# Kernel tuning notes

Measured on AMD Instinct MI355X. Metric: run time of the kernel, lower is better.

## Reference

```python
import jax, jax.numpy as jnp
import numpy as np

N_NODES = 100000
N_EDGES = 400000
F_IN = 128
HEADS = 4
C1 = 64   # conv1 out per head
C2 = 128  # conv2 out per head
G = 2048  # num graphs
FP = 2048
HID = 64
NEG_SLOPE = 0.2


def _gat_conv(x, edge_index, W, a_src, a_dst, b, heads, ch):
    """PyG-style GATConv with self-loops, concat=True."""
    n = x.shape[0]
    loops = jnp.arange(n, dtype=edge_index.dtype)
    src = jnp.concatenate([edge_index[0], loops])
    dst = jnp.concatenate([edge_index[1], loops])
    h = (x @ W).reshape(n, heads, ch)                      # [N,H,C]
    e_src = jnp.sum(h * a_src, axis=-1)                    # [N,H]
    e_dst = jnp.sum(h * a_dst, axis=-1)                    # [N,H]
    logits = jax.nn.leaky_relu(e_src[src] + e_dst[dst], NEG_SLOPE)  # [E,H]
    m = jax.ops.segment_max(logits, dst, num_segments=n)   # per-dst max
    p = jnp.exp(logits - m[dst])
    denom = jax.ops.segment_sum(p, dst, num_segments=n)
    alpha = p / denom[dst]                                 # [E,H]
    out = jax.ops.segment_sum(h[src] * alpha[:, :, None], dst, num_segments=n)
    return out.reshape(n, heads * ch) + b


def setup_inputs() -> dict:
    key = jax.random.key(0)
    ks = jax.random.split(key, 16)
    s = 0.05
    inp = {
        "x": jax.random.normal(ks[0], (N_NODES, F_IN), jnp.float32),
        "edge_index": jax.random.randint(ks[1], (2, N_EDGES), 0, N_NODES, jnp.int32),
        "batch": jnp.sort(jax.random.randint(ks[2], (N_NODES,), 0, G, jnp.int32)),
        "fp": jax.random.normal(ks[3], (G, FP), jnp.float32),
        "W1": jax.random.normal(ks[4], (F_IN, HEADS * C1), jnp.float32) * s,
        "a_src1": jax.random.normal(ks[5], (HEADS, C1), jnp.float32) * s,
        "a_dst1": jax.random.normal(ks[6], (HEADS, C1), jnp.float32) * s,
        "b1": jnp.zeros((HEADS * C1,), jnp.float32),
        "W2": jax.random.normal(ks[7], (HEADS * C1, HEADS * C2), jnp.float32) * s,
        "a_src2": jax.random.normal(ks[8], (HEADS, C2), jnp.float32) * s,
        "a_dst2": jax.random.normal(ks[9], (HEADS, C2), jnp.float32) * s,
        "b2": jnp.zeros((HEADS * C2,), jnp.float32),
        "Wfp": jax.random.normal(ks[10], (FP, HID), jnp.float32) * s,
        "bfp": jnp.zeros((HID,), jnp.float32),
        "Wfc1": jax.random.normal(ks[11], (HEADS * C2 + HID, HID), jnp.float32) * s,
        "bfc1": jnp.zeros((HID,), jnp.float32),
        "Wfc2": jax.random.normal(ks[12], (HID, 1), jnp.float32) * s,
        "bfc2": jnp.zeros((1,), jnp.float32),
    }
    return inp


def reference(x, edge_index, batch, fp, W1, a_src1, a_dst1, b1, W2, a_src2, a_dst2, b2,
              Wfp, bfp, Wfc1, bfc1, Wfc2, bfc2):
    h = _gat_conv(x, edge_index, W1, a_src1, a_dst1, b1, HEADS, C1)
    h = jax.nn.elu(h)
    h = _gat_conv(h, edge_index, W2, a_src2, a_dst2, b2, HEADS, C2)
    h = jax.nn.elu(h)
    # global mean pool over graphs
    sums = jax.ops.segment_sum(h, batch, num_segments=G)
    counts = jax.ops.segment_sum(jnp.ones((h.shape[0], 1), h.dtype), batch, num_segments=G)
    pooled = sums / jnp.maximum(counts, 1.0)               # [G, 512]
    fph = fp @ Wfp + bfp                                   # [G, 64]
    z = jnp.concatenate([pooled, fph], axis=1)             # [G, 576]
    z = jax.nn.relu(z @ Wfc1 + bfc1)
    # dropout is identity in eval mode
    return z @ Wfc2 + bfc2                                 # [G, 1]
```

## Files before the change

### kernel.cpp

```cpp
#include <hip/hip_runtime.h>
#include <math.h>

#define NEG_SLOPE 0.2f

typedef __attribute__((ext_vector_type(8))) short bf16x8;
typedef __attribute__((ext_vector_type(4))) float f32x4;

__device__ __forceinline__ float b2f(short s) {
  return __uint_as_float(((unsigned int)(unsigned short)s) << 16);
}
__device__ __forceinline__ unsigned short f2b_rne(float f) {
  unsigned int u = __float_as_uint(f);
  u = (u + 0x7FFF + ((u >> 16) & 1)) >> 16;
  return (unsigned short)u;
}

__global__ void cvt_f2b(const float* __restrict__ in, unsigned short* __restrict__ out, size_t n)
{
  size_t i = (size_t)blockIdx.x * 256 + threadIdx.x;
  size_t stride = (size_t)gridDim.x * 256;
  for (; i < n; i += stride) out[i] = f2b_rne(in[i]);
}

__global__ void transpose_f2b(const float* __restrict__ W, unsigned short* __restrict__ WT,
                              int K, int N)
{
  int idx = blockIdx.x * 256 + threadIdx.x;
  if (idx < K * N) {
    int k = idx / N, n = idx - k * N;
    WT[(size_t)n * K + k] = f2b_rne(W[idx]);
  }
}

template<int EMODE>
__global__ __launch_bounds__(256) void gemm_mfma(
    const unsigned short* __restrict__ A, const unsigned short* __restrict__ BT,
    unsigned short* __restrict__ Cout, int M, int N, int K,
    const float* __restrict__ a_src, const float* __restrict__ a_dst,
    float* __restrict__ es, float* __restrict__ ed, int nh)
{
  const int LDT = 40;
  __shared__ unsigned short As[128 * 40];
  __shared__ unsigned short Bs[128 * 40];
  const int tid  = threadIdx.x;
  const int wave = tid >> 6;
  const int lane = tid & 63;
  const int ln   = lane & 15;
  const int quad = lane >> 4;
  const int wr0  = (wave >> 1) * 64;
  const int wc0  = (wave & 1) * 64;
  const int bm   = blockIdx.y * 128;
  const int bn   = blockIdx.x * 128;
  const int srow  = tid >> 2;
  const int skoff = (tid & 3) * 8;

  f32x4 acc[4][4];
  const f32x4 z4 = {0.f, 0.f, 0.f, 0.f};
#pragma unroll
  for (int i = 0; i < 4; ++i)
#pragma unroll
    for (int j = 0; j < 4; ++j) acc[i][j] = z4;

  const bf16x8 zb8 = {0, 0, 0, 0, 0, 0, 0, 0};
  bf16x8 pa[2] = {zb8, zb8}, pb[2] = {zb8, zb8};
  bf16x8 na[2] = {zb8, zb8}, nb[2] = {zb8, zb8};
#pragma unroll
  for (int p = 0; p < 2; ++p) {
    int r = srow + p * 64;
    pa[p] = (bm + r < M) ? *(const bf16x8*)(A + (size_t)(bm + r) * K + skoff) : zb8;
    pb[p] = *(const bf16x8*)(BT + (size_t)(bn + r) * K + skoff);
  }

  for (int k0 = 0; k0 < K; k0 += 32) {
#pragma unroll
    for (int p = 0; p < 2; ++p) {
      int r = srow + p * 64;
      *(bf16x8*)(&As[r * LDT + skoff]) = pa[p];
      *(bf16x8*)(&Bs[r * LDT + skoff]) = pb[p];
    }
    __syncthreads();
    if (k0 + 32 < K) {
      int kn = k0 + 32;
#pragma unroll
      for (int p = 0; p < 2; ++p) {
        int r = srow + p * 64;
        na[p] = (bm + r < M) ? *(const bf16x8*)(A + (size_t)(bm + r) * K + kn + skoff) : zb8;
        nb[p] = *(const bf16x8*)(BT + (size_t)(bn + r) * K + kn + skoff);
      }
    }
    bf16x8 af[4], bfv[4];
#pragma unroll
    for (int i = 0; i < 4; ++i)
      af[i] = *(const bf16x8*)(&As[(wr0 + i * 16 + ln) * LDT + quad * 8]);
#pragma unroll
    for (int j = 0; j < 4; ++j)
      bfv[j] = *(const bf16x8*)(&Bs[(wc0 + j * 16 + ln) * LDT + quad * 8]);
#pragma unroll
    for (int i = 0; i < 4; ++i)
#pragma unroll
      for (int j = 0; j < 4; ++j)
        acc[i][j] = __builtin_amdgcn_mfma_f32_16x16x32_bf16(af[i], bfv[j], acc[i][j], 0, 0, 0);
    __syncthreads();
#pragma unroll
    for (int p = 0; p < 2; ++p) { pa[p] = na[p]; pb[p] = nb[p]; }
  }

#pragma unroll
  for (int i = 0; i < 4; ++i) {
#pragma unroll
    for (int r = 0; r < 4; ++r) {
      int row = bm + wr0 + i * 16 + quad * 4 + r;
      if (row >= M) continue;
#pragma unroll
      for (int j = 0; j < 4; ++j) {
        int col = bn + wc0 + j * 16 + ln;
        Cout[(size_t)row * N + col] = f2b_rne(acc[i][j][r]);
      }
    }
  }

  float asv[4], adv[4];
#pragma unroll
  for (int j = 0; j < 4; ++j) {
    int col = bn + wc0 + j * 16 + ln;
    asv[j] = a_src[col];
    adv[j] = a_dst[col];
  }
  if (EMODE == 64) {
    const int head = (bn + wc0) >> 6;
#pragma unroll
    for (int i = 0; i < 4; ++i) {
#pragma unroll
      for (int r = 0; r < 4; ++r) {
        float ps = 0.f, pd = 0.f;
#pragma unroll
        for (int j = 0; j < 4; ++j) {
          ps = fmaf(acc[i][j][r], asv[j], ps);
          pd = fmaf(acc[i][j][r], adv[j], pd);
        }
        for (int off = 8; off; off >>= 1) {
          ps += __shfl_down(ps, off, 16);
          pd += __shfl_down(pd, off, 16);
        }
        if (ln == 0) {
          int row = bm + wr0 + i * 16 + quad * 4 + r;
          if (row < M) {
            es[(size_t)row * nh + head] = ps;
            ed[(size_t)row * nh + head] = pd;
          }
        }
      }
    }
  } else {
    float* esp = (float*)As;
    float* edp = esp + 256;
#pragma unroll
    for (int i = 0; i < 4; ++i) {
#pragma unroll
      for (int r = 0; r < 4; ++r) {
        float ps = 0.f, pd = 0.f;
#pragma unroll
        for (int j = 0; j < 4; ++j) {
          ps = fmaf(acc[i][j][r], asv[j], ps);
          pd = fmaf(acc[i][j][r], adv[j], pd);
        }
        for (int off = 8; off; off >>= 1) {
          ps += __shfl_down(ps, off, 16);
          pd += __shfl_down(pd, off, 16);
        }
        if (ln == 0) {
          int rl = wr0 + i * 16 + quad * 4 + r;
          esp[rl * 2 + (wc0 >> 6)] = ps;
          edp[rl * 2 + (wc0 >> 6)] = pd;
        }
      }
    }
    __syncthreads();
    if (tid < 128) {
      int row = bm + tid;
      if (row < M) {
        int head = bn >> 7;
        es[(size_t)row * nh + head] = esp[tid * 2] + esp[tid * 2 + 1];
        ed[(size_t)row * nh + head] = edp[tid * 2] + edp[tid * 2 + 1];
      }
    }
  }
}

__global__ __launch_bounds__(256) void gemm_mfma_n64(
    const unsigned short* __restrict__ A, int lda,
    const unsigned short* __restrict__ BT, int ldb,
    float* __restrict__ Cp, int M, int kchunk)
{
  const int LDT = 72;
  __shared__ unsigned short As[128 * 72];
  __shared__ unsigned short Bs[64 * 72];
  const int tid  = threadIdx.x;
  const int wave = tid >> 6;
  const int lane = tid & 63;
  const int ln   = lane & 15;
  const int quad = lane >> 4;
  const int ks   = blockIdx.x;
  const int bm   = blockIdx.y * 128;
  const int k_beg = ks * kchunk;
  const int k_end = k_beg + kchunk;
  const int arow = tid >> 1;
  const int akb  = (tid & 1) * 32;
  const int brow = tid >> 2;
  const int bkb  = (tid & 3) * 16;

  f32x4 acc[2][4];
  const f32x4 z4 = {0.f, 0.f, 0.f, 0.f};
#pragma unroll
  for (int i = 0; i < 2; ++i)
#pragma unroll
    for (int j = 0; j < 4; ++j) acc[i][j] = z4;

  for (int k0 = k_beg; k0 < k_end; k0 += 64) {
    const unsigned short* ap = A + (size_t)(bm + arow) * lda + k0 + akb;
#pragma unroll
    for (int q = 0; q < 4; ++q)
      *(bf16x8*)(&As[arow * LDT + akb + q * 8]) = *(const bf16x8*)(ap + q * 8);
    const unsigned short* bp = BT + (size_t)brow * ldb + k0 + bkb;
#pragma unroll
    for (int q = 0; q < 2; ++q)
      *(bf16x8*)(&Bs[brow * LDT + bkb + q * 8]) = *(const bf16x8*)(bp + q * 8);
    __syncthreads();
#pragma unroll
    for (int kk = 0; kk < 2; ++kk) {
      bf16x8 af[2], bfv[4];
#pragma unroll
      for (int i = 0; i < 2; ++i)
        af[i] = *(const bf16x8*)(&As[(wave * 32 + i * 16 + ln) * LDT + kk * 32 + quad * 8]);
#pragma unroll
      for (int j = 0; j < 4; ++j)
        bfv[j] = *(const bf16x8*)(&Bs[(j * 16 + ln) * LDT + kk * 32 + quad * 8]);
#pragma unroll
      for (int i = 0; i < 2; ++i)
#pragma unroll
        for (int j = 0; j < 4; ++j)
          acc[i][j] = __builtin_amdgcn_mfma_f32_16x16x32_bf16(af[i], bfv[j], acc[i][j], 0, 0, 0);
    }
    __syncthreads();
  }
#pragma unroll
  for (int i = 0; i < 2; ++i)
#pragma unroll
    for (int r = 0; r < 4; ++r) {
      int row = bm + wave * 32 + i * 16 + quad * 4 + r;
#pragma unroll
      for (int j = 0; j < 4; ++j)
        Cp[((size_t)ks * M + row) * 64 + j * 16 + ln] = acc[i][j][r];
    }
}

__global__ void fp_finish(const float* __restrict__ Cp, int ksplit, int M,
                          const float* __restrict__ bfp,
                          unsigned short* __restrict__ zb)
{
  const int g = blockIdx.x;
  const int j = threadIdx.x;
  float s = bfp[j];
  for (int ks = 0; ks < ksplit; ++ks) s += Cp[((size_t)ks * M + g) * 64 + j];
  zb[(size_t)g * 576 + 512 + j] = f2b_rne(s);
}

__global__ void mlp_finish(const float* __restrict__ Cp, int ksplit, int M,
                           const float* __restrict__ bfc1,
                           const float* __restrict__ Wfc2, const float* __restrict__ bfc2,
                           float* __restrict__ out)
{
  const int g = blockIdx.x;
  const int j = threadIdx.x;
  float s = bfc1[j];
  for (int ks = 0; ks < ksplit; ++ks) s += Cp[((size_t)ks * M + g) * 64 + j];
  s = s > 0.f ? s : 0.f;
  float term = s * Wfc2[j];
  for (int off = 32; off; off >>= 1) term += __shfl_down(term, off, 64);
  if (j == 0) out[g] = term + bfc2[0];
}

__global__ void count_deg(const int* __restrict__ ei, int E, int* __restrict__ deg)
{
  int e = blockIdx.x * 256 + threadIdx.x;
  if (e < E) atomicAdd(&deg[ei[E + e]], 1);
}

__global__ void fill_csr(const int* __restrict__ ei, int E, int* __restrict__ cursor,
                         const int* __restrict__ rowptr, int* __restrict__ csr_src)
{
  int e = blockIdx.x * 256 + threadIdx.x;
  if (e < E) {
    int d = ei[E + e];
    int pos = atomicAdd(&cursor[d], 1);
    csr_src[rowptr[d] + pos] = ei[e];
  }
}

__global__ void count_graph(const int* __restrict__ batch, int N, int* __restrict__ gcnt)
{
  int i = blockIdx.x * 256 + threadIdx.x;
  if (i < N) atomicAdd(&gcnt[batch[i]], 1);
}

__global__ void scan_p1(const int* __restrict__ vals, int n, int* __restrict__ bsum)
{
  __shared__ int red[256];
  int base = blockIdx.x * 1024;
  int t = threadIdx.x;
  int s = 0;
#pragma unroll
  for (int i = 0; i < 4; ++i) {
    int idx = base + i * 256 + t;
    if (idx < n) s += vals[idx];
  }
  red[t] = s;
  __syncthreads();
  for (int off = 128; off; off >>= 1) {
    if (t < off) red[t] += red[t + off];
    __syncthreads();
  }
  if (t == 0) bsum[blockIdx.x] = red[0];
}

__global__ void scan_p2(const int* __restrict__ bsum, int* __restrict__ bpre,
                        int nb, int* __restrict__ rowptr, int n)
{
  __shared__ int tmp[128];
  int t = threadIdx.x;
  int v = (t < nb) ? bsum[t] : 0;
  tmp[t] = v;
  __syncthreads();
  for (int off = 1; off < 128; off <<= 1) {
    int add = (t >= off) ? tmp[t - off] : 0;
    __syncthreads();
    tmp[t] += add;
    __syncthreads();
  }
  if (t < nb) bpre[t] = tmp[t] - v;
  if (t == 127) rowptr[n] = tmp[127];
}

__global__ void scan_p3(const int* __restrict__ vals, const int* __restrict__ bpre,
                        int n, int* __restrict__ rowptr)
{
  __shared__ int tmp[256];
  int t = threadIdx.x;
  int base = blockIdx.x * 1024 + t * 4;
  int v[4]; int s = 0;
#pragma unroll
  for (int i = 0; i < 4; ++i) {
    int idx = base + i;
    v[i] = (idx < n) ? vals[idx] : 0;
    s += v[i];
  }
  tmp[t] = s;
  __syncthreads();
  for (int off = 1; off < 256; off <<= 1) {
    int add = (t >= off) ? tmp[t - off] : 0;
    __syncthreads();
    tmp[t] += add;
    __syncthreads();
  }
  int run = bpre[blockIdx.x] + tmp[t] - s;
#pragma unroll
  for (int i = 0; i < 4; ++i) {
    int idx = base + i;
    if (idx < n) rowptr[idx] = run;
    run += v[i];
  }
}

__global__ void alpha_kernel(const float* __restrict__ es, const float* __restrict__ ed,
                             const int* __restrict__ rowptr, const int* __restrict__ csr_src,
                             float* __restrict__ w_csr, float* __restrict__ wself,
                             int N, int nh)
{
  int idx = blockIdx.x * 256 + threadIdx.x;
  if (idx >= N * nh) return;
  const int dst = idx / nh;
  const int h = idx - dst * nh;
  const float edh = ed[(size_t)dst * nh + h];
  const int beg = rowptr[dst], end = rowptr[dst + 1];
  float sum = 0.f;
  for (int e = beg; e < end; ++e) {
    int s = csr_src[e];
    float l = es[(size_t)s * nh + h] + edh;
    l = l >= 0.f ? l : NEG_SLOPE * l;
    float w = expf(l);
    w_csr[(size_t)e * nh + h] = w;
    sum += w;
  }
  float ls = es[(size_t)dst * nh + h] + edh;
  ls = ls >= 0.f ? ls : NEG_SLOPE * ls;
  float wsl = expf(ls);
  sum += wsl;
  const float inv = 1.0f / sum;
  for (int e = beg; e < end; ++e) w_csr[(size_t)e * nh + h] *= inv;
  wself[(size_t)dst * nh + h] = wsl * inv;
}

__global__ __launch_bounds__(256) void aggregate_b(
    const unsigned short* __restrict__ h,
    const float* __restrict__ w_csr, const float* __restrict__ wself,
    const int* __restrict__ rowptr, const int* __restrict__ csr_src,
    const float* __restrict__ bias, unsigned short* __restrict__ out,
    int N, int nh, int C)
{
  const int HC = nh * C;
  const int CH8 = HC >> 3;
  const int dpb = 256 / CH8;
  const int grp = threadIdx.x / CH8;
  const int lane = threadIdx.x - grp * CH8;
  const int dst = blockIdx.x * dpb + grp;
  if (dst >= N) return;
  const int ch = lane << 3;
  const int head = ch / C;
  const int beg = rowptr[dst], end = rowptr[dst + 1];
  float acc[8] = {0.f, 0.f, 0.f, 0.f, 0.f, 0.f, 0.f, 0.f};
  int e = beg;
  for (; e + 1 < end; e += 2) {
    int s0 = csr_src[e], s1 = csr_src[e + 1];
    float a0 = w_csr[(size_t)e * nh + head];
    float a1 = w_csr[(size_t)(e + 1) * nh + head];
    bf16x8 h0 = *(const bf16x8*)(h + (size_t)s0 * HC + ch);
    bf16x8 h1 = *(const bf16x8*)(h + (size_t)s1 * HC + ch);
#pragma unroll
    for (int r = 0; r < 8; ++r) acc[r] = fmaf(a0, b2f(h0[r]), acc[r]);
#pragma unroll
    for (int r = 0; r < 8; ++r) acc[r] = fmaf(a1, b2f(h1[r]), acc[r]);
  }
  if (e < end) {
    int s0 = csr_src[e];
    float a0 = w_csr[(size_t)e * nh + head];
    bf16x8 h0 = *(const bf16x8*)(h + (size_t)s0 * HC + ch);
#pragma unroll
    for (int r = 0; r < 8; ++r) acc[r] = fmaf(a0, b2f(h0[r]), acc[r]);
  }
  {
    float a = wself[(size_t)dst * nh + head];
    bf16x8 hv = *(const bf16x8*)(h + (size_t)dst * HC + ch);
#pragma unroll
    for (int r = 0; r < 8; ++r) acc[r] = fmaf(a, b2f(hv[r]), acc[r]);
  }
  bf16x8 o;
#pragma unroll
  for (int r = 0; r < 8; ++r) {
    float v = acc[r] + bias[ch + r];
    v = v > 0.f ? v : (expf(v) - 1.0f);
    o[r] = (short)f2b_rne(v);
  }
  *(bf16x8*)(out + (size_t)dst * HC + ch) = o;
}

__global__ __launch_bounds__(256) void agg_pool(
    const unsigned short* __restrict__ h,
    const float* __restrict__ w_csr, const float* __restrict__ wself,
    const int* __restrict__ rowptr, const int* __restrict__ csr_src,
    const float* __restrict__ bias, const int* __restrict__ grp,
    unsigned short* __restrict__ zb)
{
  const int g = blockIdx.x;
  const int wave = threadIdx.x >> 6;
  const int lane = threadIdx.x & 63;
  const int ch = lane << 3;
  const int head = lane >> 4;
  const int gbeg = grp[g], gend = grp[g + 1];
  float bch[8];
#pragma unroll
  for (int r = 0; r < 8; ++r) bch[r] = bias[ch + r];
  float pool[8] = {0.f, 0.f, 0.f, 0.f, 0.f, 0.f, 0.f, 0.f};

  for (int node = gbeg + wave; node < gend; node += 4) {
    const int beg = rowptr[node], end = rowptr[node + 1];
    float acc[8] = {0.f, 0.f, 0.f, 0.f, 0.f, 0.f, 0.f, 0.f};
    int e = beg;
    for (; e + 1 < end; e += 2) {
      int s0 = csr_src[e], s1 = csr_src[e + 1];
      float a0 = w_csr[(size_t)e * 4 + head];
      float a1 = w_csr[(size_t)(e + 1) * 4 + head];
      bf16x8 h0 = *(const bf16x8*)(h + (size_t)s0 * 512 + ch);
      bf16x8 h1 = *(const bf16x8*)(h + (size_t)s1 * 512 + ch);
#pragma unroll
      for (int r = 0; r < 8; ++r) acc[r] = fmaf(a0, b2f(h0[r]), acc[r]);
#pragma unroll
      for (int r = 0; r < 8; ++r) acc[r] = fmaf(a1, b2f(h1[r]), acc[r]);
    }
    if (e < end) {
      int s0 = csr_src[e];
      float a0 = w_csr[(size_t)e * 4 + head];
      bf16x8 h0 = *(const bf16x8*)(h + (size_t)s0 * 512 + ch);
#pragma unroll
      for (int r = 0; r < 8; ++r) acc[r] = fmaf(a0, b2f(h0[r]), acc[r]);
    }
    {
      float a = wself[(size_t)node * 4 + head];
      bf16x8 hv = *(const bf16x8*)(h + (size_t)node * 512 + ch);
#pragma unroll
      for (int r = 0; r < 8; ++r) acc[r] = fmaf(a, b2f(hv[r]), acc[r]);
    }
#pragma unroll
    for (int r = 0; r < 8; ++r) {
      float v = acc[r] + bch[r];
      v = v > 0.f ? v : (expf(v) - 1.0f);
      pool[r] += v;
    }
  }

  __shared__ float red[4][512];
#pragma unroll
  for (int r = 0; r < 8; ++r) red[wave][ch + r] = pool[r];
  __syncthreads();
  const float inv = 1.0f / (float)max(gend - gbeg, 1);
#pragma unroll
  for (int k = 0; k < 2; ++k) {
    int c = threadIdx.x + k * 256;
    float s = (red[0][c] + red[1][c]) + (red[2][c] + red[3][c]);
    zb[(size_t)g * 576 + c] = f2b_rne(s * inv);
  }
}

extern "C" void kernel_launch(void* const* d_in, const int* in_sizes, int n_in,
                              void* d_out, int out_size, void* d_ws, size_t ws_size,
                              hipStream_t stream)
{
  const float* x      = (const float*)d_in[0];
  const int*   ei     = (const int*)d_in[1];
  const int*   batch  = (const int*)d_in[2];
  const float* fp     = (const float*)d_in[3];
  const float* W1     = (const float*)d_in[4];
  const float* a_src1 = (const float*)d_in[5];
  const float* a_dst1 = (const float*)d_in[6];
  const float* b1     = (const float*)d_in[7];
  const float* W2     = (const float*)d_in[8];
  const float* a_src2 = (const float*)d_in[9];
  const float* a_dst2 = (const float*)d_in[10];
  const float* b2     = (const float*)d_in[11];
  const float* Wfp    = (const float*)d_in[12];
  const float* bfp    = (const float*)d_in[13];
  const float* Wfc1   = (const float*)d_in[14];
  const float* bfc1   = (const float*)d_in[15];
  const float* Wfc2   = (const float*)d_in[16];
  const float* bfc2   = (const float*)d_in[17];
  float* out = (float*)d_out;

  const int NN = in_sizes[0] / 128;
  const int E  = in_sizes[1] / 2;
  const int G  = in_sizes[3] / 2048;
  const int FIN = 128, H = 4, C1 = 64, C2 = 128;
  const int HC1 = H * C1;
  const int HC2 = H * C2;
  const int KFP = in_sizes[3] / G;
  const int KZ  = HC2 + 64;
  const int KS_FP = 16;
  const int KS_Z  = 9;

  char* base = (char*)d_ws;
  size_t off = 0;
  auto alloc = [&](size_t bytes) {
    char* p = base + off; off += (bytes + 255) & ~(size_t)255; return p;
  };
  size_t xb_sz  = ((size_t)NN * FIN * 2 + 255) & ~(size_t)255;
  size_t h1b_sz = (size_t)NN * HC1 * 2;
  size_t h2b_sz = (size_t)NN * HC2 * 2;
  size_t rA = xb_sz + h1b_sz; if (h2b_sz > rA) rA = h2b_sz;
  char* RA = alloc(rA);
  unsigned short* xb  = (unsigned short*)RA;
  unsigned short* h1b = (unsigned short*)(RA + xb_sz);
  unsigned short* h2b = (unsigned short*)RA;
  size_t fpb_sz  = ((size_t)G * KFP * 2 + 255) & ~(size_t)255;
  size_t cpfp_sz = (size_t)KS_FP * G * 64 * 4;
  size_t agg1_sz = (size_t)NN * HC1 * 2;
  size_t rB = fpb_sz + cpfp_sz; if (agg1_sz > rB) rB = agg1_sz;
  char* RB = alloc(rB);
  unsigned short* fpb   = (unsigned short*)RB;
  float*          Cp_fp = (float*)(RB + fpb_sz);
  unsigned short* agg1b = (unsigned short*)RB;
  float* w1     = (float*)alloc((size_t)E * H * 4);
  float* wself1 = (float*)alloc((size_t)NN * H * 4);
  float* es1    = (float*)alloc((size_t)NN * H * 4);
  float* ed1    = (float*)alloc((size_t)NN * H * 4);
  float* w2 = w1, *wself2 = wself1, *es2 = es1, *ed2 = ed1;
  unsigned short* zb    = (unsigned short*)alloc((size_t)G * KZ * 2);
  float*          Cp_z  = (float*)alloc((size_t)KS_Z * G * 64 * 4);
  unsigned short* W1T   = (unsigned short*)alloc((size_t)HC1 * FIN * 2);
  unsigned short* W2T   = (unsigned short*)alloc((size_t)HC2 * HC1 * 2);
  unsigned short* WfpT  = (unsigned short*)alloc((size_t)64 * KFP * 2);
  unsigned short* Wfc1T = (unsigned short*)alloc((size_t)64 * KZ * 2);
  int* iarena   = (int*)alloc(((size_t)2 * NN + G) * 4);
  int* deg      = iarena;
  int* cursor   = iarena + NN;
  int* gcnt     = iarena + 2 * NN;
  int* rowptr_n = (int*)alloc(((size_t)NN + 1) * 4);
  int* rowptr_g = (int*)alloc(((size_t)G + 1) * 4);
  int* csr_src  = (int*)alloc((size_t)E * 4);
  int* bsum     = (int*)alloc(128 * 4);
  int* bpre     = (int*)alloc(128 * 4);

  {
    size_t nx = (size_t)NN * FIN;
    cvt_f2b<<<(int)((nx + 255) / 256), 256, 0, stream>>>(x, xb, nx);
    size_t nf = (size_t)G * KFP;
    cvt_f2b<<<2048, 256, 0, stream>>>(fp, fpb, nf);
    transpose_f2b<<<(FIN * HC1 + 255) / 256, 256, 0, stream>>>(W1, W1T, FIN, HC1);
    transpose_f2b<<<(HC1 * HC2 + 255) / 256, 256, 0, stream>>>(W2, W2T, HC1, HC2);
    transpose_f2b<<<(KFP * 64 + 255) / 256, 256, 0, stream>>>(Wfp, WfpT, KFP, 64);
    transpose_f2b<<<(KZ * 64 + 255) / 256, 256, 0, stream>>>(Wfc1, Wfc1T, KZ, 64);
  }

  {
    dim3 gg(KS_FP, G / 128);
    gemm_mfma_n64<<<gg, 256, 0, stream>>>(fpb, KFP, WfpT, KFP, Cp_fp, G, KFP / KS_FP);
    fp_finish<<<G, 64, 0, stream>>>(Cp_fp, KS_FP, G, bfp, zb);
  }

  hipMemsetAsync(iarena, 0, sizeof(int) * ((size_t)2 * NN + G), stream);
  count_deg<<<(E + 255) / 256, 256, 0, stream>>>(ei, E, deg);
  {
    int nb = (NN + 1023) / 1024;
    scan_p1<<<nb, 256, 0, stream>>>(deg, NN, bsum);
    scan_p2<<<1, 128, 0, stream>>>(bsum, bpre, nb, rowptr_n, NN);
    scan_p3<<<nb, 256, 0, stream>>>(deg, bpre, NN, rowptr_n);
  }
  fill_csr<<<(E + 255) / 256, 256, 0, stream>>>(ei, E, cursor, rowptr_n, csr_src);
  count_graph<<<(NN + 255) / 256, 256, 0, stream>>>(batch, NN, gcnt);
  {
    int nb = (G + 1023) / 1024;
    scan_p1<<<nb, 256, 0, stream>>>(gcnt, G, bsum);
    scan_p2<<<1, 128, 0, stream>>>(bsum, bpre, nb, rowptr_g, G);
    scan_p3<<<nb, 256, 0, stream>>>(gcnt, bpre, G, rowptr_g);
  }

  {
    dim3 gg(HC1 / 128, (NN + 127) / 128);
    gemm_mfma<64><<<gg, 256, 0, stream>>>(xb, W1T, h1b, NN, HC1, FIN,
                                          a_src1, a_dst1, es1, ed1, H);
  }
  alpha_kernel<<<(NN * H + 255) / 256, 256, 0, stream>>>(es1, ed1, rowptr_n, csr_src,
                                                         w1, wself1, NN, H);
  aggregate_b<<<(NN + 7) / 8, 256, 0, stream>>>(h1b, w1, wself1, rowptr_n, csr_src,
                                                b1, agg1b, NN, H, C1);

  {
    dim3 gg(HC2 / 128, (NN + 127) / 128);
    gemm_mfma<128><<<gg, 256, 0, stream>>>(agg1b, W2T, h2b, NN, HC2, HC1,
                                           a_src2, a_dst2, es2, ed2, H);
  }
  alpha_kernel<<<(NN * H + 255) / 256, 256, 0, stream>>>(es2, ed2, rowptr_n, csr_src,
                                                         w2, wself2, NN, H);
  agg_pool<<<G, 256, 0, stream>>>(h2b, w2, wself2, rowptr_n, csr_src, b2, rowptr_g, zb);

  {
    dim3 gg(KS_Z, G / 128);
    gemm_mfma_n64<<<gg, 256, 0, stream>>>(zb, KZ, Wfc1T, KZ, Cp_z, G, KZ / KS_Z);
    mlp_finish<<<G, 64, 0, stream>>>(Cp_z, KS_Z, G, bfc1, Wfc2, bfc2, out);
  }
}
```

Measured before the change: 520.9 us.

## Defer softmax normalization to aggregation and split feature channels across grid.y

The alpha kernel no longer rescales every edge weight by the inverse denominator. It stores only the unnormalized weights plus a per-node inverse sum, and the aggregation kernels multiply the accumulated result by that inverse, removing a second read-modify-write pass over the edge weights. Both aggregation kernels also split the feature channels into two halves along grid.y, so each block covers more nodes with fewer channels, giving more parallelism per graph in the pooling kernel. The cost is an extra per-node buffer and gathered source rows being read by two blocks instead of one.

```diff
diff --git a/kernel.cpp b/kernel.cpp
--- a/kernel.cpp
+++ b/kernel.cpp
@@ -374,7 +374,7 @@
 __global__ void alpha_kernel(const float* __restrict__ es, const float* __restrict__ ed,
                              const int* __restrict__ rowptr, const int* __restrict__ csr_src,
                              float* __restrict__ w_csr, float* __restrict__ wself,
-                             int N, int nh)
+                             float* __restrict__ dinv, int N, int nh)
 {
   int idx = blockIdx.x * 256 + threadIdx.x;
   if (idx >= N * nh) return;
@@ -395,34 +395,32 @@
   ls = ls >= 0.f ? ls : NEG_SLOPE * ls;
   float wsl = expf(ls);
   sum += wsl;
-  const float inv = 1.0f / sum;
-  for (int e = beg; e < end; ++e) w_csr[(size_t)e * nh + h] *= inv;
-  wself[(size_t)dst * nh + h] = wsl * inv;
+  wself[(size_t)dst * nh + h] = wsl;
+  dinv[(size_t)dst * nh + h] = 1.0f / sum;
 }
 
 __global__ __launch_bounds__(256) void aggregate_b(
     const unsigned short* __restrict__ h,
     const float* __restrict__ w_csr, const float* __restrict__ wself,
+    const float* __restrict__ dinv,
     const int* __restrict__ rowptr, const int* __restrict__ csr_src,
-    const float* __restrict__ bias, unsigned short* __restrict__ out,
-    int N, int nh, int C)
-{
-  const int HC = nh * C;
-  const int CH8 = HC >> 3;
-  const int dpb = 256 / CH8;
-  const int grp = threadIdx.x / CH8;
-  const int lane = threadIdx.x - grp * CH8;
-  const int dst = blockIdx.x * dpb + grp;
+    const float* __restrict__ bias, unsigned short* __restrict__ out, int N)
+{
+  const int HC = 256;
+  const int p = blockIdx.y;
+  const int grp = threadIdx.x >> 4;
+  const int l16 = threadIdx.x & 15;
+  const int dst = blockIdx.x * 16 + grp;
   if (dst >= N) return;
-  const int ch = lane << 3;
-  const int head = ch / C;
+  const int ch = p * 128 + l16 * 8;
+  const int head = ch >> 6;
   const int beg = rowptr[dst], end = rowptr[dst + 1];
   float acc[8] = {0.f, 0.f, 0.f, 0.f, 0.f, 0.f, 0.f, 0.f};
   int e = beg;
   for (; e + 1 < end; e += 2) {
     int s0 = csr_src[e], s1 = csr_src[e + 1];
-    float a0 = w_csr[(size_t)e * nh + head];
-    float a1 = w_csr[(size_t)(e + 1) * nh + head];
+    float a0 = w_csr[(size_t)e * 4 + head];
+    float a1 = w_csr[(size_t)(e + 1) * 4 + head];
     bf16x8 h0 = *(const bf16x8*)(h + (size_t)s0 * HC + ch);
     bf16x8 h1 = *(const bf16x8*)(h + (size_t)s1 * HC + ch);
 #pragma unroll
@@ -432,21 +430,22 @@
   }
   if (e < end) {
     int s0 = csr_src[e];
-    float a0 = w_csr[(size_t)e * nh + head];
+    float a0 = w_csr[(size_t)e * 4 + head];
     bf16x8 h0 = *(const bf16x8*)(h + (size_t)s0 * HC + ch);
 #pragma unroll
     for (int r = 0; r < 8; ++r) acc[r] = fmaf(a0, b2f(h0[r]), acc[r]);
   }
   {
-    float a = wself[(size_t)dst * nh + head];
+    float a = wself[(size_t)dst * 4 + head];
     bf16x8 hv = *(const bf16x8*)(h + (size_t)dst * HC + ch);
 #pragma unroll
     for (int r = 0; r < 8; ++r) acc[r] = fmaf(a, b2f(hv[r]), acc[r]);
   }
+  const float di = dinv[(size_t)dst * 4 + head];
   bf16x8 o;
 #pragma unroll
   for (int r = 0; r < 8; ++r) {
-    float v = acc[r] + bias[ch + r];
+    float v = acc[r] * di + bias[ch + r];
     v = v > 0.f ? v : (expf(v) - 1.0f);
     o[r] = (short)f2b_rne(v);
   }
@@ -456,22 +455,27 @@
 __global__ __launch_bounds__(256) void agg_pool(
     const unsigned short* __restrict__ h,
     const float* __restrict__ w_csr, const float* __restrict__ wself,
+    const float* __restrict__ dinv,
     const int* __restrict__ rowptr, const int* __restrict__ csr_src,
     const float* __restrict__ bias, const int* __restrict__ grp,
     unsigned short* __restrict__ zb)
 {
   const int g = blockIdx.x;
+  const int p = blockIdx.y;
   const int wave = threadIdx.x >> 6;
   const int lane = threadIdx.x & 63;
-  const int ch = lane << 3;
-  const int head = lane >> 4;
+  const int lg   = lane >> 5;
+  const int ll   = lane & 31;
+  const int ch   = p * 256 + ll * 8;
+  const int head = ch >> 7;
+  const int slot = wave * 2 + lg;
   const int gbeg = grp[g], gend = grp[g + 1];
   float bch[8];
 #pragma unroll
   for (int r = 0; r < 8; ++r) bch[r] = bias[ch + r];
   float pool[8] = {0.f, 0.f, 0.f, 0.f, 0.f, 0.f, 0.f, 0.f};
 
-  for (int node = gbeg + wave; node < gend; node += 4) {
+  for (int node = gbeg + slot; node < gend; node += 8) {
     const int beg = rowptr[node], end = rowptr[node + 1];
     float acc[8] = {0.f, 0.f, 0.f, 0.f, 0.f, 0.f, 0.f, 0.f};
     int e = beg;
@@ -499,24 +503,25 @@
 #pragma unroll
       for (int r = 0; r < 8; ++r) acc[r] = fmaf(a, b2f(hv[r]), acc[r]);
     }
+    const float di = dinv[(size_t)node * 4 + head];
 #pragma unroll
     for (int r = 0; r < 8; ++r) {
-      float v = acc[r] + bch[r];
+      float v = acc[r] * di + bch[r];
       v = v > 0.f ? v : (expf(v) - 1.0f);
       pool[r] += v;
     }
   }
 
-  __shared__ float red[4][512];
-#pragma unroll
-  for (int r = 0; r < 8; ++r) red[wave][ch + r] = pool[r];
+  __shared__ float red[8][256];
+#pragma unroll
+  for (int r = 0; r < 8; ++r) red[slot][ll * 8 + r] = pool[r];
   __syncthreads();
   const float inv = 1.0f / (float)max(gend - gbeg, 1);
-#pragma unroll
-  for (int k = 0; k < 2; ++k) {
-    int c = threadIdx.x + k * 256;
-    float s = (red[0][c] + red[1][c]) + (red[2][c] + red[3][c]);
-    zb[(size_t)g * 576 + c] = f2b_rne(s * inv);
+  {
+    int c = threadIdx.x;
+    float s = ((red[0][c] + red[1][c]) + (red[2][c] + red[3][c]))
+            + ((red[4][c] + red[5][c]) + (red[6][c] + red[7][c]));
+    zb[(size_t)g * 576 + p * 256 + c] = f2b_rne(s * inv);
   }
 }
 
@@ -580,7 +585,8 @@
   float* wself1 = (float*)alloc((size_t)NN * H * 4);
   float* es1    = (float*)alloc((size_t)NN * H * 4);
   float* ed1    = (float*)alloc((size_t)NN * H * 4);
-  float* w2 = w1, *wself2 = wself1, *es2 = es1, *ed2 = ed1;
+  float* dinv1  = (float*)alloc((size_t)NN * H * 4);
+  float* w2 = w1, *wself2 = wself1, *es2 = es1, *ed2 = ed1, *dinv2 = dinv1;
   unsigned short* zb    = (unsigned short*)alloc((size_t)G * KZ * 2);
   float*          Cp_z  = (float*)alloc((size_t)KS_Z * G * 64 * 4);
   unsigned short* W1T   = (unsigned short*)alloc((size_t)HC1 * FIN * 2);
@@ -637,9 +643,12 @@
                                           a_src1, a_dst1, es1, ed1, H);
   }
   alpha_kernel<<<(NN * H + 255) / 256, 256, 0, stream>>>(es1, ed1, rowptr_n, csr_src,
-                                                         w1, wself1, NN, H);
-  aggregate_b<<<(NN + 7) / 8, 256, 0, stream>>>(h1b, w1, wself1, rowptr_n, csr_src,
-                                                b1, agg1b, NN, H, C1);
+                                                         w1, wself1, dinv1, NN, H);
+  {
+    dim3 gg((NN + 15) / 16, 2);
+    aggregate_b<<<gg, 256, 0, stream>>>(h1b, w1, wself1, dinv1, rowptr_n, csr_src,
+                                        b1, agg1b, NN);
+  }
 
   {
     dim3 gg(HC2 / 128, (NN + 127) / 128);
@@ -647,8 +656,12 @@
                                            a_src2, a_dst2, es2, ed2, H);
   }
   alpha_kernel<<<(NN * H + 255) / 256, 256, 0, stream>>>(es2, ed2, rowptr_n, csr_src,
-                                                         w2, wself2, NN, H);
-  agg_pool<<<G, 256, 0, stream>>>(h2b, w2, wself2, rowptr_n, csr_src, b2, rowptr_g, zb);
+                                                         w2, wself2, dinv2, NN, H);
+  {
+    dim3 gg(G, 2);
+    agg_pool<<<gg, 256, 0, stream>>>(h2b, w2, wself2, dinv2, rowptr_n, csr_src,
+                                     b2, rowptr_g, zb);
+  }
 
   {
     dim3 gg(KS_Z, G / 128);
```

After: 516.2 us. About the same (-0.9%).

## Merge prep, count and scan launches; defer softmax normalization to aggregation

Applied to the files above, without the earlier changes.

Folds the six conversion/transpose launches into one prep_all kernel, and merges the degree and graph-count kernels and the two three-pass scans into combined launches. The alpha kernel no longer rescales every edge weight in a second pass. It stores the unnormalized self weight plus a per-destination reciprocal sum, which the aggregation kernels apply once per output. This removes launch overhead and one read-modify-write pass over the edge weights, at the cost of an extra small buffer read in aggregation.

```diff
diff --git a/kernel.cpp b/kernel.cpp
--- a/kernel.cpp
+++ b/kernel.cpp
@@ -15,21 +15,45 @@
   return (unsigned short)u;
 }
 
-__global__ void cvt_f2b(const float* __restrict__ in, unsigned short* __restrict__ out, size_t n)
-{
-  size_t i = (size_t)blockIdx.x * 256 + threadIdx.x;
-  size_t stride = (size_t)gridDim.x * 256;
-  for (; i < n; i += stride) out[i] = f2b_rne(in[i]);
-}
-
-__global__ void transpose_f2b(const float* __restrict__ W, unsigned short* __restrict__ WT,
-                              int K, int N)
-{
-  int idx = blockIdx.x * 256 + threadIdx.x;
+__device__ __forceinline__ void tr_one(const float* __restrict__ W,
+                                       unsigned short* __restrict__ WT,
+                                       int K, int N, int idx)
+{
   if (idx < K * N) {
     int k = idx / N, n = idx - k * N;
     WT[(size_t)n * K + k] = f2b_rne(W[idx]);
   }
+}
+
+__global__ __launch_bounds__(256) void prep_all(
+    const float* __restrict__ x, unsigned short* __restrict__ xb, size_t nx, int B0,
+    const float* __restrict__ fp, unsigned short* __restrict__ fpb, size_t nf, int B1,
+    const float* __restrict__ W1, unsigned short* __restrict__ W1T,
+    const float* __restrict__ W2, unsigned short* __restrict__ W2T,
+    const float* __restrict__ Wfp, unsigned short* __restrict__ WfpT,
+    const float* __restrict__ Wfc1, unsigned short* __restrict__ Wfc1T)
+{
+  int b = blockIdx.x;
+  const int t = threadIdx.x;
+  if (b < B0) {
+    size_t i = (size_t)b * 256 + t;
+    if (i < nx) xb[i] = f2b_rne(x[i]);
+    return;
+  }
+  b -= B0;
+  if (b < B1) {
+    size_t i = (size_t)b * 256 + t;
+    if (i < nf) fpb[i] = f2b_rne(fp[i]);
+    return;
+  }
+  b -= B1;
+  if (b < 128) { tr_one(W1, W1T, 128, 256, b * 256 + t); return; }
+  b -= 128;
+  if (b < 512) { tr_one(W2, W2T, 256, 512, b * 256 + t); return; }
+  b -= 512;
+  if (b < 512) { tr_one(Wfp, WfpT, 2048, 64, b * 256 + t); return; }
+  b -= 512;
+  tr_one(Wfc1, Wfc1T, 576, 64, b * 256 + t);
 }
 
 template<int EMODE>
@@ -280,10 +304,19 @@
   if (j == 0) out[g] = term + bfc2[0];
 }
 
-__global__ void count_deg(const int* __restrict__ ei, int E, int* __restrict__ deg)
-{
-  int e = blockIdx.x * 256 + threadIdx.x;
-  if (e < E) atomicAdd(&deg[ei[E + e]], 1);
+__global__ void count_all(const int* __restrict__ ei, int E, int* __restrict__ deg,
+                          const int* __restrict__ batch, int NN, int* __restrict__ gcnt,
+                          int BE)
+{
+  int b = blockIdx.x;
+  int t = threadIdx.x;
+  if (b < BE) {
+    int e = b * 256 + t;
+    if (e < E) atomicAdd(&deg[ei[E + e]], 1);
+  } else {
+    int i = (b - BE) * 256 + t;
+    if (i < NN) atomicAdd(&gcnt[batch[i]], 1);
+  }
 }
 
 __global__ void fill_csr(const int* __restrict__ ei, int E, int* __restrict__ cursor,
@@ -297,16 +330,11 @@
   }
 }
 
-__global__ void count_graph(const int* __restrict__ batch, int N, int* __restrict__ gcnt)
-{
-  int i = blockIdx.x * 256 + threadIdx.x;
-  if (i < N) atomicAdd(&gcnt[batch[i]], 1);
-}
-
-__global__ void scan_p1(const int* __restrict__ vals, int n, int* __restrict__ bsum)
+__device__ void scan_p1_body(const int* __restrict__ vals, int n, int* __restrict__ bsum,
+                             int bb)
 {
   __shared__ int red[256];
-  int base = blockIdx.x * 1024;
+  int base = bb * 1024;
   int t = threadIdx.x;
   int s = 0;
 #pragma unroll
@@ -320,11 +348,19 @@
     if (t < off) red[t] += red[t + off];
     __syncthreads();
   }
-  if (t == 0) bsum[blockIdx.x] = red[0];
-}
-
-__global__ void scan_p2(const int* __restrict__ bsum, int* __restrict__ bpre,
-                        int nb, int* __restrict__ rowptr, int n)
+  if (t == 0) bsum[bb] = red[0];
+}
+
+__global__ void scan2_p1(const int* __restrict__ vA, int nA, int* __restrict__ bsA, int nbA,
+                         const int* __restrict__ vB, int nB, int* __restrict__ bsB)
+{
+  int b = blockIdx.x;
+  if (b < nbA) scan_p1_body(vA, nA, bsA, b);
+  else         scan_p1_body(vB, nB, bsB, b - nbA);
+}
+
+__device__ void scan_p2_body(const int* __restrict__ bsum, int* __restrict__ bpre,
+                             int nb, int* __restrict__ rowptr, int n)
 {
   __shared__ int tmp[128];
   int t = threadIdx.x;
@@ -341,12 +377,21 @@
   if (t == 127) rowptr[n] = tmp[127];
 }
 
-__global__ void scan_p3(const int* __restrict__ vals, const int* __restrict__ bpre,
-                        int n, int* __restrict__ rowptr)
+__global__ void scan2_p2(const int* __restrict__ bsA, int* __restrict__ bpA, int nbA,
+                         int* __restrict__ rpA, int nA,
+                         const int* __restrict__ bsB, int* __restrict__ bpB, int nbB,
+                         int* __restrict__ rpB, int nB)
+{
+  if (blockIdx.x == 0) scan_p2_body(bsA, bpA, nbA, rpA, nA);
+  else                 scan_p2_body(bsB, bpB, nbB, rpB, nB);
+}
+
+__device__ void scan_p3_body(const int* __restrict__ vals, const int* __restrict__ bpre,
+                             int n, int* __restrict__ rowptr, int bb)
 {
   __shared__ int tmp[256];
   int t = threadIdx.x;
-  int base = blockIdx.x * 1024 + t * 4;
+  int base = bb * 1024 + t * 4;
   int v[4]; int s = 0;
 #pragma unroll
   for (int i = 0; i < 4; ++i) {
@@ -362,7 +407,7 @@
     tmp[t] += add;
     __syncthreads();
   }
-  int run = bpre[blockIdx.x] + tmp[t] - s;
+  int run = bpre[bb] + tmp[t] - s;
 #pragma unroll
   for (int i = 0; i < 4; ++i) {
     int idx = base + i;
@@ -371,10 +416,20 @@
   }
 }
 
+__global__ void scan2_p3(const int* __restrict__ vA, const int* __restrict__ bpA, int nA,
+                         int* __restrict__ rpA, int nbA,
+                         const int* __restrict__ vB, const int* __restrict__ bpB, int nB,
+                         int* __restrict__ rpB)
+{
+  int b = blockIdx.x;
+  if (b < nbA) scan_p3_body(vA, bpA, nA, rpA, b);
+  else         scan_p3_body(vB, bpB, nB, rpB, b - nbA);
+}
+
 __global__ void alpha_kernel(const float* __restrict__ es, const float* __restrict__ ed,
                              const int* __restrict__ rowptr, const int* __restrict__ csr_src,
                              float* __restrict__ w_csr, float* __restrict__ wself,
-                             int N, int nh)
+                             float* __restrict__ dinv, int N, int nh)
 {
   int idx = blockIdx.x * 256 + threadIdx.x;
   if (idx >= N * nh) return;
@@ -395,14 +450,14 @@
   ls = ls >= 0.f ? ls : NEG_SLOPE * ls;
   float wsl = expf(ls);
   sum += wsl;
-  const float inv = 1.0f / sum;
-  for (int e = beg; e < end; ++e) w_csr[(size_t)e * nh + h] *= inv;
-  wself[(size_t)dst * nh + h] = wsl * inv;
+  wself[(size_t)dst * nh + h] = wsl;
+  dinv[(size_t)dst * nh + h] = 1.0f / sum;
 }
 
 __global__ __launch_bounds__(256) void aggregate_b(
     const unsigned short* __restrict__ h,
     const float* __restrict__ w_csr, const float* __restrict__ wself,
+    const float* __restrict__ dinv,
     const int* __restrict__ rowptr, const int* __restrict__ csr_src,
     const float* __restrict__ bias, unsigned short* __restrict__ out,
     int N, int nh, int C)
@@ -443,10 +498,11 @@
 #pragma unroll
     for (int r = 0; r < 8; ++r) acc[r] = fmaf(a, b2f(hv[r]), acc[r]);
   }
+  const float di = dinv[(size_t)dst * nh + head];
   bf16x8 o;
 #pragma unroll
   for (int r = 0; r < 8; ++r) {
-    float v = acc[r] + bias[ch + r];
+    float v = acc[r] * di + bias[ch + r];
     v = v > 0.f ? v : (expf(v) - 1.0f);
     o[r] = (short)f2b_rne(v);
   }
@@ -456,6 +512,7 @@
 __global__ __launch_bounds__(256) void agg_pool(
     const unsigned short* __restrict__ h,
     const float* __restrict__ w_csr, const float* __restrict__ wself,
+    const float* __restrict__ dinv,
     const int* __restrict__ rowptr, const int* __restrict__ csr_src,
     const float* __restrict__ bias, const int* __restrict__ grp,
     unsigned short* __restrict__ zb)
@@ -499,9 +556,10 @@
 #pragma unroll
       for (int r = 0; r < 8; ++r) acc[r] = fmaf(a, b2f(hv[r]), acc[r]);
     }
+    const float di = dinv[(size_t)node * 4 + head];
 #pragma unroll
     for (int r = 0; r < 8; ++r) {
-      float v = acc[r] + bch[r];
+      float v = acc[r] * di + bch[r];
       v = v > 0.f ? v : (expf(v) - 1.0f);
       pool[r] += v;
     }
@@ -580,7 +638,8 @@
   float* wself1 = (float*)alloc((size_t)NN * H * 4);
   float* es1    = (float*)alloc((size_t)NN * H * 4);
   float* ed1    = (float*)alloc((size_t)NN * H * 4);
-  float* w2 = w1, *wself2 = wself1, *es2 = es1, *ed2 = ed1;
+  float* dinv1  = (float*)alloc((size_t)NN * H * 4);
+  float* w2 = w1, *wself2 = wself1, *es2 = es1, *ed2 = ed1, *dinv2 = dinv1;
   unsigned short* zb    = (unsigned short*)alloc((size_t)G * KZ * 2);
   float*          Cp_z  = (float*)alloc((size_t)KS_Z * G * 64 * 4);
   unsigned short* W1T   = (unsigned short*)alloc((size_t)HC1 * FIN * 2);
@@ -594,18 +653,19 @@
   int* rowptr_n = (int*)alloc(((size_t)NN + 1) * 4);
   int* rowptr_g = (int*)alloc(((size_t)G + 1) * 4);
   int* csr_src  = (int*)alloc((size_t)E * 4);
-  int* bsum     = (int*)alloc(128 * 4);
-  int* bpre     = (int*)alloc(128 * 4);
-
+  int* bsumA    = (int*)alloc(128 * 4);
+  int* bpreA    = (int*)alloc(128 * 4);
+  int* bsumB    = (int*)alloc(128 * 4);
+  int* bpreB    = (int*)alloc(128 * 4);
+
+  const size_t nx = (size_t)NN * FIN;
+  const size_t nf = (size_t)G * KFP;
+  const int B0 = (int)((nx + 255) / 256);
+  const int B1 = (int)((nf + 255) / 256);
   {
-    size_t nx = (size_t)NN * FIN;
-    cvt_f2b<<<(int)((nx + 255) / 256), 256, 0, stream>>>(x, xb, nx);
-    size_t nf = (size_t)G * KFP;
-    cvt_f2b<<<2048, 256, 0, stream>>>(fp, fpb, nf);
-    transpose_f2b<<<(FIN * HC1 + 255) / 256, 256, 0, stream>>>(W1, W1T, FIN, HC1);
-    transpose_f2b<<<(HC1 * HC2 + 255) / 256, 256, 0, stream>>>(W2, W2T, HC1, HC2);
-    transpose_f2b<<<(KFP * 64 + 255) / 256, 256, 0, stream>>>(Wfp, WfpT, KFP, 64);
-    transpose_f2b<<<(KZ * 64 + 255) / 256, 256, 0, stream>>>(Wfc1, Wfc1T, KZ, 64);
+    int nb = B0 + B1 + 128 + 512 + 512 + 144;
+    prep_all<<<nb, 256, 0, stream>>>(x, xb, nx, B0, fp, fpb, nf, B1,
+                                     W1, W1T, W2, W2T, Wfp, WfpT, Wfc1, Wfc1T);
   }
 
   {
@@ -615,21 +675,21 @@
   }
 
   hipMemsetAsync(iarena, 0, sizeof(int) * ((size_t)2 * NN + G), stream);
-  count_deg<<<(E + 255) / 256, 256, 0, stream>>>(ei, E, deg);
   {
-    int nb = (NN + 1023) / 1024;
-    scan_p1<<<nb, 256, 0, stream>>>(deg, NN, bsum);
-    scan_p2<<<1, 128, 0, stream>>>(bsum, bpre, nb, rowptr_n, NN);
-    scan_p3<<<nb, 256, 0, stream>>>(deg, bpre, NN, rowptr_n);
+    int BE = (E + 255) / 256;
+    int BN = (NN + 255) / 256;
+    count_all<<<BE + BN, 256, 0, stream>>>(ei, E, deg, batch, NN, gcnt, BE);
+  }
+  {
+    int nbA = (NN + 1023) / 1024;
+    int nbB = (G + 1023) / 1024;
+    scan2_p1<<<nbA + nbB, 256, 0, stream>>>(deg, NN, bsumA, nbA, gcnt, G, bsumB);
+    scan2_p2<<<2, 128, 0, stream>>>(bsumA, bpreA, nbA, rowptr_n, NN,
+                                    bsumB, bpreB, nbB, rowptr_g, G);
+    scan2_p3<<<nbA + nbB, 256, 0, stream>>>(deg, bpreA, NN, rowptr_n, nbA,
+                                            gcnt, bpreB, G, rowptr_g);
   }
   fill_csr<<<(E + 255) / 256, 256, 0, stream>>>(ei, E, cursor, rowptr_n, csr_src);
-  count_graph<<<(NN + 255) / 256, 256, 0, stream>>>(batch, NN, gcnt);
-  {
-    int nb = (G + 1023) / 1024;
-    scan_p1<<<nb, 256, 0, stream>>>(gcnt, G, bsum);
-    scan_p2<<<1, 128, 0, stream>>>(bsum, bpre, nb, rowptr_g, G);
-    scan_p3<<<nb, 256, 0, stream>>>(gcnt, bpre, G, rowptr_g);
-  }
 
   {
     dim3 gg(HC1 / 128, (NN + 127) / 128);
@@ -637,8 +697,8 @@
                                           a_src1, a_dst1, es1, ed1, H);
   }
   alpha_kernel<<<(NN * H + 255) / 256, 256, 0, stream>>>(es1, ed1, rowptr_n, csr_src,
-                                                         w1, wself1, NN, H);
-  aggregate_b<<<(NN + 7) / 8, 256, 0, stream>>>(h1b, w1, wself1, rowptr_n, csr_src,
+                                                         w1, wself1, dinv1, NN, H);
+  aggregate_b<<<(NN + 7) / 8, 256, 0, stream>>>(h1b, w1, wself1, dinv1, rowptr_n, csr_src,
                                                 b1, agg1b, NN, H, C1);
 
   {
@@ -647,8 +707,9 @@
                                            a_src2, a_dst2, es2, ed2, H);
   }
   alpha_kernel<<<(NN * H + 255) / 256, 256, 0, stream>>>(es2, ed2, rowptr_n, csr_src,
-                                                         w2, wself2, NN, H);
-  agg_pool<<<G, 256, 0, stream>>>(h2b, w2, wself2, rowptr_n, csr_src, b2, rowptr_g, zb);
+                                                         w2, wself2, dinv2, NN, H);
+  agg_pool<<<G, 256, 0, stream>>>(h2b, w2, wself2, dinv2, rowptr_n, csr_src,
+                                  b2, rowptr_g, zb);
 
   {
     dim3 gg(KS_Z, G / 128);
```

Result: faster. 492.3 us (-5.5%).
